# Kernel tuning notes

Hardware: AMD Instinct MI355X
Metric: run time of the kernel (lower is better)

The kernel has to match this reference:

```python
import jax, jax.numpy as jnp
import numpy as np

BLOCK_SIZE = 128
N_OUT = 4096
K_IN = 4096


def setup_inputs() -> dict:
    key = jax.random.key(0)
    k_x, k_w, k_s = jax.random.split(key, 3)
    x = jax.random.normal(k_x, (1, 1024, K_IN), dtype=jnp.float32)
    # ternary weights stored as int8 in {-2,-1,0,+1} (zero-point subtracted)
    weight_q = (jax.random.randint(k_w, (N_OUT, K_IN), 0, 4) - 2).astype(jnp.int8)
    n_blocks = K_IN // BLOCK_SIZE
    scales = jax.random.uniform(k_s, (N_OUT, n_blocks), dtype=jnp.float32) * 0.1 + 0.01
    return {"x": x, "weight_q": weight_q, "scales": scales}


def reference(x, weight_q, scales):
    N, K = weight_q.shape
    n_blocks = K // BLOCK_SIZE
    orig_shape = x.shape
    # [tokens, n_blocks, block_size]
    x_blocked = x.reshape(-1, n_blocks, BLOCK_SIZE).astype(jnp.float32)
    # [N, n_blocks, block_size]
    w_blocked = weight_q.reshape(N, n_blocks, BLOCK_SIZE).astype(jnp.float32)
    # per-block partial dot products: [tokens, N, n_blocks]
    raw = jnp.einsum('bki,nki->bnk', x_blocked, w_blocked)
    # apply per-(out_feature, block) scale then reduce over blocks
    out = (raw * scales).sum(axis=-1)  # [tokens, N]
    return out.astype(x.dtype).reshape(*orig_shape[:-1], N)
```

## Files before the change

### kernel.cpp

```cpp
#include <hip/hip_runtime.h>
#include <stdint.h>


#define MM 1024
#define NN 4096
#define KK 4096
#define BK 128

typedef __attribute__((ext_vector_type(4))) int intx4;
typedef __attribute__((ext_vector_type(16))) int intx16;
typedef __attribute__((ext_vector_type(4))) float floatx4;
typedef __attribute__((ext_vector_type(16))) float floatx16;

typedef const __attribute__((address_space(1))) void global_cvoid;
typedef __attribute__((address_space(3))) void lds_void;

__global__ __launch_bounds__(256) void prep(const float* __restrict__ x,
                                            const int* __restrict__ wq,
                                            char* __restrict__ xq,
                                            float* __restrict__ qrow,
                                            char* __restrict__ wb) {
    const int tid = threadIdx.x;
    if (blockIdx.x < MM) {
        const int m = blockIdx.x;
        const float* xr = x + (size_t)m * KK;
        floatx4 v[4];
        float amax = 0.f;
#pragma unroll
        for (int c = 0; c < 4; ++c) {
            v[c] = *(const floatx4*)(xr + (c * 256 + tid) * 4);
#pragma unroll
            for (int e = 0; e < 4; ++e) amax = fmaxf(amax, fabsf(v[c][e]));
        }
#pragma unroll
        for (int off = 32; off; off >>= 1) amax = fmaxf(amax, __shfl_down(amax, off));
        __shared__ float wmax[4];
        if ((tid & 63) == 0) wmax[tid >> 6] = amax;
        __syncthreads();
        amax = fmaxf(fmaxf(wmax[0], wmax[1]), fmaxf(wmax[2], wmax[3]));
        amax = fmaxf(amax, 1e-20f);
        const float qinv = 127.0f / amax;
        if (tid == 0) qrow[m] = amax / 127.0f;
#pragma unroll
        for (int c = 0; c < 4; ++c) {
            int p = 0;
#pragma unroll
            for (int e = 0; e < 4; ++e) {
                float r = rintf(v[c][e] * qinv);
                r = fminf(fmaxf(r, -127.f), 127.f);
                p |= ((int)r & 255) << (8 * e);
            }
            *(int*)(xq + (size_t)m * KK + (c * 256 + tid) * 4) = p;
        }
    } else {
        const int blk = blockIdx.x - MM;
#pragma unroll
        for (int c = 0; c < 4; ++c) {
            size_t c4 = (size_t)blk * 1024 + c * 256 + tid;
            intx4 a = ((const intx4*)wq)[c4];
            ((int*)wb)[c4] = (a[0] & 255) | ((a[1] & 255) << 8) |
                             ((a[2] & 255) << 16) | (a[3] << 24);
        }
    }
}

__global__ __launch_bounds__(256, 2) void q8_gemm(const char* __restrict__ xq,
                                                  const char* __restrict__ wb,
                                                  const float* __restrict__ qrow,
                                                  const float* __restrict__ scales,
                                                  float* __restrict__ out) {
    __shared__ char As[2][64 * BK];
    __shared__ char Bs[2][128 * BK];
    __shared__ float Sl[128 * 33];

    const int tid  = threadIdx.x;
    const int lane = tid & 63;
    const int wave = tid >> 6;
    const int l31  = lane & 31;
    const int hi   = lane >> 5;
    const int sw   = lane & 7;
    const int wn   = wave * 32;

    const int bid = blockIdx.x;
    const int xcd = bid & 7, loc = bid >> 3;
    const int nT = xcd * 4 + (loc & 3);
    const int mT = loc >> 2;
    const int mBase = mT * 64, nBase = nT * 128;

    const int rg = lane >> 3;
    const int cs = (lane & 7) ^ rg;
    const char* gA = xq + (size_t)(mBase + wave * 16 + rg) * KK + cs * 16;
    const char* gB = wb + (size_t)(nBase + wave * 32 + rg) * KK + cs * 16;
    const int ldsRowA = wave * 16;
    const int ldsRowB = wave * 32;

    floatx16 fac0, fac1;
#pragma unroll
    for (int r = 0; r < 16; ++r) { fac0[r] = 0.f; fac1[r] = 0.f; }

#define STAGE(BUF, SLAB)                                                        \
    {                                                                           \
        _Pragma("unroll")                                                       \
        for (int t = 0; t < 2; ++t)                                             \
            __builtin_amdgcn_global_load_lds(                                   \
                (global_cvoid*)(gA + (size_t)(t * 8) * KK + (SLAB) * BK),       \
                (lds_void*)&As[BUF][(ldsRowA + t * 8) * BK], 16, 0, 0);         \
        _Pragma("unroll")                                                       \
        for (int t = 0; t < 4; ++t)                                             \
            __builtin_amdgcn_global_load_lds(                                   \
                (global_cvoid*)(gB + (size_t)(t * 8) * KK + (SLAB) * BK),       \
                (lds_void*)&Bs[BUF][(ldsRowB + t * 8) * BK], 16, 0, 0);         \
    }

#define COMPUTE(BUF, SLAB)                                                      \
    {                                                                           \
        const float sf = Sl[(wn + l31) * 33 + (SLAB)];                          \
        intx16 iacc0, iacc1;                                                    \
        __builtin_amdgcn_s_setprio(1);                                          \
        _Pragma("unroll")                                                       \
        for (int kp = 0; kp < 4; ++kp) {                                        \
            const int kc = (((kp * 2) + hi) ^ sw) << 4;                         \
            intx4 av0 = *(const intx4*)&As[BUF][l31 * BK + kc];                 \
            intx4 av1 = *(const intx4*)&As[BUF][(32 + l31) * BK + kc];          \
            intx4 bv  = *(const intx4*)&Bs[BUF][(wn + l31) * BK + kc];          \
            if (kp == 0) {                                                      \
                intx16 z = {0, 0, 0, 0, 0, 0, 0, 0, 0, 0, 0, 0, 0, 0, 0, 0};    \
                iacc0 = __builtin_amdgcn_mfma_i32_32x32x32_i8(av0, bv, z, 0, 0, 0); \
                iacc1 = __builtin_amdgcn_mfma_i32_32x32x32_i8(av1, bv, z, 0, 0, 0); \
            } else {                                                            \
                iacc0 = __builtin_amdgcn_mfma_i32_32x32x32_i8(av0, bv, iacc0, 0, 0, 0); \
                iacc1 = __builtin_amdgcn_mfma_i32_32x32x32_i8(av1, bv, iacc1, 0, 0, 0); \
            }                                                                   \
        }                                                                       \
        __builtin_amdgcn_s_setprio(0);                                          \
        _Pragma("unroll")                                                       \
        for (int r = 0; r < 16; ++r) {                                          \
            fac0[r] += (float)iacc0[r] * sf;                                    \
            fac1[r] += (float)iacc1[r] * sf;                                    \
        }                                                                       \
    }

    STAGE(0, 0)
    for (int t = tid; t < 4096; t += 256) {
        int nl = t >> 5, b = t & 31;
        Sl[nl * 33 + b] = scales[(size_t)(nBase + nl) * 32 + b];
    }
    __syncthreads();

    const int NIT = KK / BK;
    for (int it = 0; it < NIT; it += 2) {
        if (it + 1 < NIT) STAGE(1, it + 1)
        COMPUTE(0, it)
        __syncthreads();
        if (it + 2 < NIT) STAGE(0, it + 2)
        COMPUTE(1, it + 1)
        __syncthreads();
    }

#pragma unroll
    for (int g = 0; g < 4; ++g) {
        floatx4 qv0 = *(const floatx4*)(qrow + mBase + g * 8 + hi * 4);
        floatx4 qv1 = *(const floatx4*)(qrow + mBase + 32 + g * 8 + hi * 4);
#pragma unroll
        for (int r = 0; r < 4; ++r) {
            const int m0 = mBase + g * 8 + hi * 4 + r;
            out[(size_t)m0 * NN + nBase + wn + l31]        = fac0[g * 4 + r] * qv0[r];
            out[(size_t)(m0 + 32) * NN + nBase + wn + l31] = fac1[g * 4 + r] * qv1[r];
        }
    }
#undef STAGE
#undef COMPUTE
}

extern "C" void kernel_launch(void* const* d_in, const int* in_sizes, int n_in,
                              void* d_out, int out_size, void* d_ws, size_t ws_size,
                              hipStream_t stream) {
    const float* x      = (const float*)d_in[0];
    const int*   wq     = (const int*)d_in[1];
    const float* scales = (const float*)d_in[2];
    float*       out    = (float*)d_out;

    char*  xq   = (char*)d_ws;
    float* qrow = (float*)((char*)d_ws + (size_t)MM * KK);
    char*  wb   = (char*)d_ws + (size_t)MM * KK + 4096;

    prep<<<MM + (size_t)NN * KK / 16 / 256, 256, 0, stream>>>(x, wq, xq, qrow, wb);
    q8_gemm<<<(MM / 64) * (NN / 128), 256, 0, stream>>>(xq, wb, qrow, scales, out);
}
```

Baseline: 144.1 us.

## Load B operand directly from global into registers, bypassing LDS

Each wave's B tile is used only by that wave, so the weight slab is now loaded straight from global memory into registers with a double-buffered register prefetch. The LDS Bs buffers and their global_load_lds staging are removed. This cuts LDS footprint and LDS read traffic and may raise occupancy, at the cost of more VGPRs and per-lane strided global loads that may coalesce less well. The K ordering of B (hi*16 + kp*32) has to match A's swizzled kc order for the result to stay correct.

```diff
diff --git a/kernel.cpp b/kernel.cpp
--- a/kernel.cpp
+++ b/kernel.cpp
@@ -70,7 +70,6 @@
                                                   const float* __restrict__ scales,
                                                   float* __restrict__ out) {
     __shared__ char As[2][64 * BK];
-    __shared__ char Bs[2][128 * BK];
     __shared__ float Sl[128 * 33];
 
     const int tid  = threadIdx.x;
@@ -90,29 +89,31 @@
     const int rg = lane >> 3;
     const int cs = (lane & 7) ^ rg;
     const char* gA = xq + (size_t)(mBase + wave * 16 + rg) * KK + cs * 16;
-    const char* gB = wb + (size_t)(nBase + wave * 32 + rg) * KK + cs * 16;
     const int ldsRowA = wave * 16;
-    const int ldsRowB = wave * 32;
+
+    const char* gBrow = wb + (size_t)(nBase + wn + l31) * KK + hi * 16;
 
     floatx16 fac0, fac1;
 #pragma unroll
     for (int r = 0; r < 16; ++r) { fac0[r] = 0.f; fac1[r] = 0.f; }
 
-#define STAGE(BUF, SLAB)                                                        \
+#define STAGE_A(BUF, SLAB)                                                      \
     {                                                                           \
         _Pragma("unroll")                                                       \
         for (int t = 0; t < 2; ++t)                                             \
             __builtin_amdgcn_global_load_lds(                                   \
                 (global_cvoid*)(gA + (size_t)(t * 8) * KK + (SLAB) * BK),       \
                 (lds_void*)&As[BUF][(ldsRowA + t * 8) * BK], 16, 0, 0);         \
-        _Pragma("unroll")                                                       \
-        for (int t = 0; t < 4; ++t)                                             \
-            __builtin_amdgcn_global_load_lds(                                   \
-                (global_cvoid*)(gB + (size_t)(t * 8) * KK + (SLAB) * BK),       \
-                (lds_void*)&Bs[BUF][(ldsRowB + t * 8) * BK], 16, 0, 0);         \
     }
 
-#define COMPUTE(BUF, SLAB)                                                      \
+#define LOAD_B(BV, SLAB)                                                        \
+    {                                                                           \
+        _Pragma("unroll")                                                       \
+        for (int kp = 0; kp < 4; ++kp)                                          \
+            BV[kp] = *(const intx4*)(gBrow + (size_t)(SLAB) * BK + kp * 32);    \
+    }
+
+#define COMPUTE(BUF, SLAB, BV)                                                  \
     {                                                                           \
         const float sf = Sl[(wn + l31) * 33 + (SLAB)];                          \
         intx16 iacc0, iacc1;                                                    \
@@ -122,14 +123,15 @@
             const int kc = (((kp * 2) + hi) ^ sw) << 4;                         \
             intx4 av0 = *(const intx4*)&As[BUF][l31 * BK + kc];                 \
             intx4 av1 = *(const intx4*)&As[BUF][(32 + l31) * BK + kc];          \
-            intx4 bv  = *(const intx4*)&Bs[BUF][(wn + l31) * BK + kc];          \
+            const int kq = ((kp * 2) + hi) >> 1;    \
+            (void)kq;                                                           \
             if (kp == 0) {                                                      \
                 intx16 z = {0, 0, 0, 0, 0, 0, 0, 0, 0, 0, 0, 0, 0, 0, 0, 0};    \
-                iacc0 = __builtin_amdgcn_mfma_i32_32x32x32_i8(av0, bv, z, 0, 0, 0); \
-                iacc1 = __builtin_amdgcn_mfma_i32_32x32x32_i8(av1, bv, z, 0, 0, 0); \
+                iacc0 = __builtin_amdgcn_mfma_i32_32x32x32_i8(av0, BV[kp], z, 0, 0, 0); \
+                iacc1 = __builtin_amdgcn_mfma_i32_32x32x32_i8(av1, BV[kp], z, 0, 0, 0); \
             } else {                                                            \
-                iacc0 = __builtin_amdgcn_mfma_i32_32x32x32_i8(av0, bv, iacc0, 0, 0, 0); \
-                iacc1 = __builtin_amdgcn_mfma_i32_32x32x32_i8(av1, bv, iacc1, 0, 0, 0); \
+                iacc0 = __builtin_amdgcn_mfma_i32_32x32x32_i8(av0, BV[kp], iacc0, 0, 0, 0); \
+                iacc1 = __builtin_amdgcn_mfma_i32_32x32x32_i8(av1, BV[kp], iacc1, 0, 0, 0); \
             }                                                                   \
         }                                                                       \
         __builtin_amdgcn_s_setprio(0);                                          \
@@ -140,7 +142,10 @@
         }                                                                       \
     }
 
-    STAGE(0, 0)
+
+    intx4 bvA[4], bvB[4];
+    STAGE_A(0, 0)
+    LOAD_B(bvA, 0)
     for (int t = tid; t < 4096; t += 256) {
         int nl = t >> 5, b = t & 31;
         Sl[nl * 33 + b] = scales[(size_t)(nBase + nl) * 32 + b];
@@ -149,11 +154,11 @@
 
     const int NIT = KK / BK;
     for (int it = 0; it < NIT; it += 2) {
-        if (it + 1 < NIT) STAGE(1, it + 1)
-        COMPUTE(0, it)
+        if (it + 1 < NIT) { STAGE_A(1, it + 1) LOAD_B(bvB, it + 1) }
+        COMPUTE(0, it, bvA)
         __syncthreads();
-        if (it + 2 < NIT) STAGE(0, it + 2)
-        COMPUTE(1, it + 1)
+        if (it + 2 < NIT) { STAGE_A(0, it + 2) LOAD_B(bvA, it + 2) }
+        COMPUTE(1, it + 1, bvB)
         __syncthreads();
     }
 
@@ -168,7 +173,8 @@
             out[(size_t)(m0 + 32) * NN + nBase + wn + l31] = fac1[g * 4 + r] * qv1[r];
         }
     }
-#undef STAGE
+#undef STAGE_A
+#undef LOAD_B
 #undef COMPUTE
 }
 
```

New measurement: 151.9 us. 1.05x slower.

## Triple-buffer GEMM K-loop with explicit vmcnt waits and per-lane scale prefetch

Applied to the files above, without the earlier changes.

Replaces the double-buffered LDS pipeline with a three-stage ring, so two slabs of A/B are in flight while one is computed. Synchronisation now uses explicit vmcnt waits and raw s_barriers, and all LDS fragments are read into registers before the next DMA is issued into the freed buffer. The per-block LDS scale table is dropped in favour of per-lane scalar scale loads, prefetched one stage ahead. This aims to hide global-load latency and cut the prologue, at the cost of more LDS (48KB), more registers, and hand-tuned waitcnt values that must match the count of outstanding loads.

```diff
diff --git a/kernel.cpp b/kernel.cpp
--- a/kernel.cpp
+++ b/kernel.cpp
@@ -69,9 +69,8 @@
                                                   const float* __restrict__ qrow,
                                                   const float* __restrict__ scales,
                                                   float* __restrict__ out) {
-    __shared__ char As[2][64 * BK];
-    __shared__ char Bs[2][128 * BK];
-    __shared__ float Sl[128 * 33];
+    __shared__ char As[3][64 * BK];
+    __shared__ char Bs[3][128 * BK];
 
     const int tid  = threadIdx.x;
     const int lane = tid & 63;
@@ -94,68 +93,84 @@
     const int ldsRowA = wave * 16;
     const int ldsRowB = wave * 32;
 
+    const float* scrow = scales + (size_t)(nBase + wn + l31) * 32;
+
     floatx16 fac0, fac1;
 #pragma unroll
     for (int r = 0; r < 16; ++r) { fac0[r] = 0.f; fac1[r] = 0.f; }
 
-#define STAGE(BUF, SLAB)                                                        \
+#define STAGE_DMA(BUF, SLAB)                                                    \
     {                                                                           \
         _Pragma("unroll")                                                       \
         for (int t = 0; t < 2; ++t)                                             \
             __builtin_amdgcn_global_load_lds(                                   \
-                (global_cvoid*)(gA + (size_t)(t * 8) * KK + (SLAB) * BK),       \
+                (global_cvoid*)(gA + (size_t)(t * 8) * KK + (size_t)(SLAB) * BK),\
                 (lds_void*)&As[BUF][(ldsRowA + t * 8) * BK], 16, 0, 0);         \
         _Pragma("unroll")                                                       \
         for (int t = 0; t < 4; ++t)                                             \
             __builtin_amdgcn_global_load_lds(                                   \
-                (global_cvoid*)(gB + (size_t)(t * 8) * KK + (SLAB) * BK),       \
+                (global_cvoid*)(gB + (size_t)(t * 8) * KK + (size_t)(SLAB) * BK),\
                 (lds_void*)&Bs[BUF][(ldsRowB + t * 8) * BK], 16, 0, 0);         \
     }
 
-#define COMPUTE(BUF, SLAB)                                                      \
+#define STEP(BUF, WAITN, DO_STAGE, JNXT, SC)                                    \
     {                                                                           \
-        const float sf = Sl[(wn + l31) * 33 + (SLAB)];                          \
+        asm volatile("s_waitcnt vmcnt(" #WAITN ")" ::: "memory");               \
+        __builtin_amdgcn_s_barrier();                                           \
+        intx4 av0[4], av1[4], bv[4];                                            \
+        _Pragma("unroll")                                                       \
+        for (int kp = 0; kp < 4; ++kp) {                                        \
+            const int kc = (((kp * 2) + hi) ^ sw) << 4;                         \
+            av0[kp] = *(const intx4*)&As[BUF][l31 * BK + kc];                   \
+            av1[kp] = *(const intx4*)&As[BUF][(32 + l31) * BK + kc];            \
+            bv[kp]  = *(const intx4*)&Bs[BUF][(wn + l31) * BK + kc];            \
+        }                                                                       \
+        asm volatile("s_waitcnt lgkmcnt(0)" ::: "memory");                      \
+        __builtin_amdgcn_sched_barrier(0);                                      \
+        __builtin_amdgcn_s_barrier();                                           \
+        if (DO_STAGE) { STAGE_DMA(BUF, JNXT) }                                  \
+        asm volatile("" ::: "memory");                                          \
         intx16 iacc0, iacc1;                                                    \
         __builtin_amdgcn_s_setprio(1);                                          \
         _Pragma("unroll")                                                       \
         for (int kp = 0; kp < 4; ++kp) {                                        \
-            const int kc = (((kp * 2) + hi) ^ sw) << 4;                         \
-            intx4 av0 = *(const intx4*)&As[BUF][l31 * BK + kc];                 \
-            intx4 av1 = *(const intx4*)&As[BUF][(32 + l31) * BK + kc];          \
-            intx4 bv  = *(const intx4*)&Bs[BUF][(wn + l31) * BK + kc];          \
             if (kp == 0) {                                                      \
                 intx16 z = {0, 0, 0, 0, 0, 0, 0, 0, 0, 0, 0, 0, 0, 0, 0, 0};    \
-                iacc0 = __builtin_amdgcn_mfma_i32_32x32x32_i8(av0, bv, z, 0, 0, 0); \
-                iacc1 = __builtin_amdgcn_mfma_i32_32x32x32_i8(av1, bv, z, 0, 0, 0); \
+                iacc0 = __builtin_amdgcn_mfma_i32_32x32x32_i8(av0[0], bv[0], z, 0, 0, 0); \
+                iacc1 = __builtin_amdgcn_mfma_i32_32x32x32_i8(av1[0], bv[0], z, 0, 0, 0); \
             } else {                                                            \
-                iacc0 = __builtin_amdgcn_mfma_i32_32x32x32_i8(av0, bv, iacc0, 0, 0, 0); \
-                iacc1 = __builtin_amdgcn_mfma_i32_32x32x32_i8(av1, bv, iacc1, 0, 0, 0); \
+                iacc0 = __builtin_amdgcn_mfma_i32_32x32x32_i8(av0[kp], bv[kp], iacc0, 0, 0, 0); \
+                iacc1 = __builtin_amdgcn_mfma_i32_32x32x32_i8(av1[kp], bv[kp], iacc1, 0, 0, 0); \
             }                                                                   \
         }                                                                       \
         __builtin_amdgcn_s_setprio(0);                                          \
         _Pragma("unroll")                                                       \
         for (int r = 0; r < 16; ++r) {                                          \
-            fac0[r] += (float)iacc0[r] * sf;                                    \
-            fac1[r] += (float)iacc1[r] * sf;                                    \
+            fac0[r] += (float)iacc0[r] * (SC);                                  \
+            fac1[r] += (float)iacc1[r] * (SC);                                  \
         }                                                                       \
-    }
-
-    STAGE(0, 0)
-    for (int t = tid; t < 4096; t += 256) {
-        int nl = t >> 5, b = t & 31;
-        Sl[nl * 33 + b] = scales[(size_t)(nBase + nl) * 32 + b];
-    }
-    __syncthreads();
-
-    const int NIT = KK / BK;
-    for (int it = 0; it < NIT; it += 2) {
-        if (it + 1 < NIT) STAGE(1, it + 1)
-        COMPUTE(0, it)
-        __syncthreads();
-        if (it + 2 < NIT) STAGE(0, it + 2)
-        COMPUTE(1, it + 1)
-        __syncthreads();
-    }
+        if (DO_STAGE) { SC = scrow[(JNXT)]; }                                   \
+        asm volatile("" ::: "memory");                                          \
+    }
+
+    float sc0, sc1, sc2;
+    STAGE_DMA(0, 0) sc0 = scrow[0];
+    asm volatile("" ::: "memory");
+    STAGE_DMA(1, 1) sc1 = scrow[1];
+    asm volatile("" ::: "memory");
+    STAGE_DMA(2, 2) sc2 = scrow[2];
+    asm volatile("" ::: "memory");
+
+    for (int base = 0; base < 27; base += 3) {
+        STEP(0, 14, 1, base + 3, sc0)
+        STEP(1, 14, 1, base + 4, sc1)
+        STEP(2, 14, 1, base + 5, sc2)
+    }
+    STEP(0, 14, 1, 30, sc0)
+    STEP(1, 14, 1, 31, sc1)
+    STEP(2, 14, 0, 0, sc2)
+    STEP(0, 7, 0, 0, sc0)
+    STEP(1, 0, 0, 0, sc1)
 
 #pragma unroll
     for (int g = 0; g < 4; ++g) {
@@ -168,8 +183,8 @@
             out[(size_t)(m0 + 32) * NN + nBase + wn + l31] = fac1[g * 4 + r] * qv1[r];
         }
     }
-#undef STAGE
-#undef COMPUTE
+#undef STAGE_DMA
+#undef STEP
 }
 
 extern "C" void kernel_launch(void* const* d_in, const int* in_sizes, int n_in,
```

New measurement: 146.2 us. No clear change (+1.5%).

## Shrink GEMM tile to 64x64 with 2x2 wave layout and register scales

Applied to the files above, without the earlier changes.

The output tile per block shrinks from 64x128 to 64x64, and the four waves are arranged 2x2 so each computes one 32x32 MFMA tile instead of two. The launch count doubles and the occupancy hint rises to four blocks per CU. The LDS scale table and its preload are removed; per-slab scales are read straight from global memory into registers and prefetched one slab ahead. This cuts LDS use and registers per wave to allow more concurrent blocks, at the cost of lower data reuse per block (more global and L2 traffic for A) and fewer MFMAs per LDS load.

```diff
diff --git a/kernel.cpp b/kernel.cpp
--- a/kernel.cpp
+++ b/kernel.cpp
@@ -64,14 +64,13 @@
     }
 }
 
-__global__ __launch_bounds__(256, 2) void q8_gemm(const char* __restrict__ xq,
+__global__ __launch_bounds__(256, 4) void q8_gemm(const char* __restrict__ xq,
                                                   const char* __restrict__ wb,
                                                   const float* __restrict__ qrow,
                                                   const float* __restrict__ scales,
                                                   float* __restrict__ out) {
     __shared__ char As[2][64 * BK];
-    __shared__ char Bs[2][128 * BK];
-    __shared__ float Sl[128 * 33];
+    __shared__ char Bs[2][64 * BK];
 
     const int tid  = threadIdx.x;
     const int lane = tid & 63;
@@ -79,93 +78,83 @@
     const int l31  = lane & 31;
     const int hi   = lane >> 5;
     const int sw   = lane & 7;
-    const int wn   = wave * 32;
+    const int wm   = wave >> 1;
+    const int wn2  = wave & 1;
 
     const int bid = blockIdx.x;
     const int xcd = bid & 7, loc = bid >> 3;
-    const int nT = xcd * 4 + (loc & 3);
-    const int mT = loc >> 2;
-    const int mBase = mT * 64, nBase = nT * 128;
+    const int nT = xcd * 8 + (loc & 7);
+    const int mT = loc >> 3;
+    const int mBase = mT * 64, nBase = nT * 64;
 
     const int rg = lane >> 3;
     const int cs = (lane & 7) ^ rg;
     const char* gA = xq + (size_t)(mBase + wave * 16 + rg) * KK + cs * 16;
-    const char* gB = wb + (size_t)(nBase + wave * 32 + rg) * KK + cs * 16;
-    const int ldsRowA = wave * 16;
-    const int ldsRowB = wave * 32;
+    const char* gB = wb + (size_t)(nBase + wave * 16 + rg) * KK + cs * 16;
+    const int ldsRow = wave * 16;
 
-    floatx16 fac0, fac1;
+    const float* scrow = scales + (size_t)(nBase + wn2 * 32 + l31) * 32;
+
+    floatx16 fac;
 #pragma unroll
-    for (int r = 0; r < 16; ++r) { fac0[r] = 0.f; fac1[r] = 0.f; }
+    for (int r = 0; r < 16; ++r) fac[r] = 0.f;
 
 #define STAGE(BUF, SLAB)                                                        \
     {                                                                           \
         _Pragma("unroll")                                                       \
         for (int t = 0; t < 2; ++t)                                             \
             __builtin_amdgcn_global_load_lds(                                   \
-                (global_cvoid*)(gA + (size_t)(t * 8) * KK + (SLAB) * BK),       \
-                (lds_void*)&As[BUF][(ldsRowA + t * 8) * BK], 16, 0, 0);         \
+                (global_cvoid*)(gA + (size_t)(t * 8) * KK + (size_t)(SLAB) * BK),\
+                (lds_void*)&As[BUF][(ldsRow + t * 8) * BK], 16, 0, 0);          \
         _Pragma("unroll")                                                       \
-        for (int t = 0; t < 4; ++t)                                             \
+        for (int t = 0; t < 2; ++t)                                             \
             __builtin_amdgcn_global_load_lds(                                   \
-                (global_cvoid*)(gB + (size_t)(t * 8) * KK + (SLAB) * BK),       \
-                (lds_void*)&Bs[BUF][(ldsRowB + t * 8) * BK], 16, 0, 0);         \
+                (global_cvoid*)(gB + (size_t)(t * 8) * KK + (size_t)(SLAB) * BK),\
+                (lds_void*)&Bs[BUF][(ldsRow + t * 8) * BK], 16, 0, 0);          \
     }
 
-#define COMPUTE(BUF, SLAB)                                                      \
+#define COMPUTE(BUF, SF)                                                        \
     {                                                                           \
-        const float sf = Sl[(wn + l31) * 33 + (SLAB)];                          \
-        intx16 iacc0, iacc1;                                                    \
+        intx16 iacc;                                                            \
         __builtin_amdgcn_s_setprio(1);                                          \
         _Pragma("unroll")                                                       \
         for (int kp = 0; kp < 4; ++kp) {                                        \
             const int kc = (((kp * 2) + hi) ^ sw) << 4;                         \
-            intx4 av0 = *(const intx4*)&As[BUF][l31 * BK + kc];                 \
-            intx4 av1 = *(const intx4*)&As[BUF][(32 + l31) * BK + kc];          \
-            intx4 bv  = *(const intx4*)&Bs[BUF][(wn + l31) * BK + kc];          \
+            intx4 av = *(const intx4*)&As[BUF][(wm * 32 + l31) * BK + kc];      \
+            intx4 bv = *(const intx4*)&Bs[BUF][(wn2 * 32 + l31) * BK + kc];     \
             if (kp == 0) {                                                      \
                 intx16 z = {0, 0, 0, 0, 0, 0, 0, 0, 0, 0, 0, 0, 0, 0, 0, 0};    \
-                iacc0 = __builtin_amdgcn_mfma_i32_32x32x32_i8(av0, bv, z, 0, 0, 0); \
-                iacc1 = __builtin_amdgcn_mfma_i32_32x32x32_i8(av1, bv, z, 0, 0, 0); \
+                iacc = __builtin_amdgcn_mfma_i32_32x32x32_i8(av, bv, z, 0, 0, 0); \
             } else {                                                            \
-                iacc0 = __builtin_amdgcn_mfma_i32_32x32x32_i8(av0, bv, iacc0, 0, 0, 0); \
-                iacc1 = __builtin_amdgcn_mfma_i32_32x32x32_i8(av1, bv, iacc1, 0, 0, 0); \
+                iacc = __builtin_amdgcn_mfma_i32_32x32x32_i8(av, bv, iacc, 0, 0, 0); \
             }                                                                   \
         }                                                                       \
         __builtin_amdgcn_s_setprio(0);                                          \
         _Pragma("unroll")                                                       \
-        for (int r = 0; r < 16; ++r) {                                          \
-            fac0[r] += (float)iacc0[r] * sf;                                    \
-            fac1[r] += (float)iacc1[r] * sf;                                    \
-        }                                                                       \
+        for (int r = 0; r < 16; ++r) fac[r] += (float)iacc[r] * (SF);           \
     }
 
+    float sfA = scrow[0], sfB;
     STAGE(0, 0)
-    for (int t = tid; t < 4096; t += 256) {
-        int nl = t >> 5, b = t & 31;
-        Sl[nl * 33 + b] = scales[(size_t)(nBase + nl) * 32 + b];
-    }
     __syncthreads();
 
     const int NIT = KK / BK;
     for (int it = 0; it < NIT; it += 2) {
-        if (it + 1 < NIT) STAGE(1, it + 1)
-        COMPUTE(0, it)
+        if (it + 1 < NIT) { STAGE(1, it + 1) sfB = scrow[it + 1]; }
+        COMPUTE(0, sfA)
         __syncthreads();
-        if (it + 2 < NIT) STAGE(0, it + 2)
-        COMPUTE(1, it + 1)
+        if (it + 2 < NIT) { STAGE(0, it + 2) sfA = scrow[it + 2]; }
+        COMPUTE(1, sfB)
         __syncthreads();
     }
 
 #pragma unroll
     for (int g = 0; g < 4; ++g) {
-        floatx4 qv0 = *(const floatx4*)(qrow + mBase + g * 8 + hi * 4);
-        floatx4 qv1 = *(const floatx4*)(qrow + mBase + 32 + g * 8 + hi * 4);
+        floatx4 qv = *(const floatx4*)(qrow + mBase + wm * 32 + g * 8 + hi * 4);
 #pragma unroll
         for (int r = 0; r < 4; ++r) {
-            const int m0 = mBase + g * 8 + hi * 4 + r;
-            out[(size_t)m0 * NN + nBase + wn + l31]        = fac0[g * 4 + r] * qv0[r];
-            out[(size_t)(m0 + 32) * NN + nBase + wn + l31] = fac1[g * 4 + r] * qv1[r];
+            const int m0 = mBase + wm * 32 + g * 8 + hi * 4 + r;
+            out[(size_t)m0 * NN + nBase + wn2 * 32 + l31] = fac[g * 4 + r] * qv[r];
         }
     }
 #undef STAGE
@@ -185,5 +174,5 @@
     char*  wb   = (char*)d_ws + (size_t)MM * KK + 4096;
 
     prep<<<MM + (size_t)NN * KK / 16 / 256, 256, 0, stream>>>(x, wq, xq, qrow, wb);
-    q8_gemm<<<(MM / 64) * (NN / 128), 256, 0, stream>>>(xq, wb, qrow, scales, out);
+    q8_gemm<<<(MM / 64) * (NN / 64), 256, 0, stream>>>(xq, wb, qrow, scales, out);
 }
```

After: 150.6 us. 1.05x slower.
